# Kernel optimization log

Measured on AMD Instinct MI355X. Metric: run time of the kernel, lower is better.

Reference implementation:

```python
import jax, jax.numpy as jnp
import numpy as np

B, T, V, E_DIM, H = 1024, 512, 8, 32, 64  # batch, seq_len, num_actions, embed_dim, hidden_dim


def setup_inputs() -> dict:
    key = jax.random.key(0)
    ks = jax.random.split(key, 12)
    s = lambda k, shape: jax.random.normal(k, shape, dtype=jnp.float32) * 0.1
    return {
        "x": jax.random.randint(ks[0], (B, T), 0, V),
        "emb": s(ks[1], (V, E_DIM)),
        # PyTorch LSTM layer 0: weight_ih [4H, E], weight_hh [4H, H], biases [4H]
        "Wih0": s(ks[2], (4 * H, E_DIM)), "Whh0": s(ks[3], (4 * H, H)),
        "bih0": s(ks[4], (4 * H,)), "bhh0": s(ks[5], (4 * H,)),
        # layer 1: input size H
        "Wih1": s(ks[6], (4 * H, H)), "Whh1": s(ks[7], (4 * H, H)),
        "bih1": s(ks[8], (4 * H,)), "bhh1": s(ks[9], (4 * H,)),
        "Wfc": s(ks[10], (V, H)), "bfc": s(ks[11], (V,)),
    }


def _lstm_layer(x, Wih, Whh, bih, bhh):
    """Single LSTM layer, batch_first input x: [B, T, in] -> [B, T, H].
    PyTorch gate order: i, f, g, o."""
    Bsz = x.shape[0]
    Hd = Whh.shape[1]
    # precompute input contribution for all timesteps in one GEMM: [B, T, 4H]
    x_gates = jnp.einsum('bti,gi->btg', x, Wih) + bih + bhh

    def step(carry, xg):
        h, c = carry
        gates = xg + h @ Whh.T  # [B, 4H]
        i, f, g, o = jnp.split(gates, 4, axis=-1)
        i = jax.nn.sigmoid(i)
        f = jax.nn.sigmoid(f)
        g = jnp.tanh(g)
        o = jax.nn.sigmoid(o)
        c = f * c + i * g
        h = o * jnp.tanh(c)
        return (h, c), h

    h0 = jnp.zeros((Bsz, Hd), x.dtype)
    (_, _), hs = jax.lax.scan(step, (h0, h0), jnp.swapaxes(x_gates, 0, 1))
    return jnp.swapaxes(hs, 0, 1)  # [B, T, H]


def reference(x, emb, Wih0, Whh0, bih0, bhh0, Wih1, Whh1, bih1, bhh1, Wfc, bfc):
    # embedding lookup
    e = emb[x]  # [B, T, E]
    # 2-layer LSTM (dropout between layers / before fc is identity in eval mode)
    h1 = _lstm_layer(e, Wih0, Whh0, bih0, bhh0)
    h2 = _lstm_layer(h1, Wih1, Whh1, bih1, bhh1)
    last = h2[:, -1, :]  # [B, H]
    logits = last @ Wfc.T + bfc  # [B, V]
    return logits
```

## Files before the change

### kernel.cpp

```cpp
#include <hip/hip_runtime.h>

#define Bsz   1024
#define Tlen  512
#define VOC   8
#define EDIM  32
#define HDIM  64
#define G4    256
#define SEQB  4
#define NT    512
#define NBLK  (Bsz / SEQB)
#define ITERS 520

typedef _Float16 f16x8 __attribute__((ext_vector_type(8)));
typedef float    f32x4 __attribute__((ext_vector_type(4)));

__device__ __forceinline__ float ex2(float x) {
#if __has_builtin(__builtin_amdgcn_exp2f)
    return __builtin_amdgcn_exp2f(x);
#else
    return exp2f(x);
#endif
}
__device__ __forceinline__ float rcp_(float x) {
#if __has_builtin(__builtin_amdgcn_rcpf)
    return __builtin_amdgcn_rcpf(x);
#else
    return 1.0f / x;
#endif
}

__device__ __forceinline__ void cell_upd(float ai, float af, float ag, float ao,
                                         float& c, float& h) {
    const float K1 = 1.4426950408889634f;
    float ei = ex2(fminf(-K1 * ai, 60.0f));
    float ef = ex2(fminf(-K1 * af, 60.0f));
    float eg = ex2(fminf(-2.0f * K1 * ag, 60.0f));
    float eo = ex2(fminf(-K1 * ao, 60.0f));
    float di = 1.0f + ei, df = 1.0f + ef, dg = 1.0f + eg, dn = 1.0f + eo;
    float r1 = rcp_(di * df);
    float si = df * r1;
    float sf = di * r1;
    float r2 = rcp_(dg * dn);
    float tg = __builtin_fmaf(2.0f * dn, r2, -1.0f);
    float so = dg * r2;
    c = sf * c + si * tg;
    float ec = ex2(fminf(-2.0f * K1 * c, 60.0f));
    h = so * __builtin_fmaf(2.0f, rcp_(1.0f + ec), -1.0f);
}

__global__ void precompute_kernel(const float* __restrict__ emb,
                                  const float* __restrict__ Wih0,
                                  const float* __restrict__ bih0,
                                  const float* __restrict__ bhh0,
                                  const float* __restrict__ bih1,
                                  const float* __restrict__ bhh1,
                                  float* __restrict__ ws) {
    int g = threadIdx.x;
    int v = blockIdx.x;
    if (v < VOC) {
        float acc = bih0[g] + bhh0[g];
        #pragma unroll
        for (int e = 0; e < EDIM; ++e)
            acc += Wih0[g * EDIM + e] * emb[v * EDIM + e];
        const int q = g >> 6, c = g & 63;
        ws[(v * 64 + c) * 4 + q] = acc;
    } else {
        ws[VOC * G4 + g] = bih1[g] + bhh1[g];
    }
}

__device__ __forceinline__ f16x8 read_h_frag(const _Float16* hb, int kc, int l) {
    int off = kc * 512 + ((l * 8) ^ ((l & 3) << 7));
    return *(const f16x8*)(hb + off);
}
__device__ __forceinline__ void write_h(_Float16* hb, int r, int c, float v) {
    int off = (c >> 5) * 512 +
              (((((c & 31) >> 3) * 128) + r * 8 + (c & 7)) ^ ((r & 3) << 7));
    hb[off] = (_Float16)v;
}

#define MFMA8(A0, A1, W0, W1, C0, C1, C2, C3)                                   \
    C0 = __builtin_amdgcn_mfma_f32_16x16x32_f16(A0, W0[0], C0, 0, 0, 0);        \
    C1 = __builtin_amdgcn_mfma_f32_16x16x32_f16(A0, W0[1], C1, 0, 0, 0);        \
    C2 = __builtin_amdgcn_mfma_f32_16x16x32_f16(A0, W0[2], C2, 0, 0, 0);        \
    C3 = __builtin_amdgcn_mfma_f32_16x16x32_f16(A0, W0[3], C3, 0, 0, 0);        \
    C0 = __builtin_amdgcn_mfma_f32_16x16x32_f16(A1, W1[0], C0, 0, 0, 0);        \
    C1 = __builtin_amdgcn_mfma_f32_16x16x32_f16(A1, W1[1], C1, 0, 0, 0);        \
    C2 = __builtin_amdgcn_mfma_f32_16x16x32_f16(A1, W1[2], C2, 0, 0, 0);        \
    C3 = __builtin_amdgcn_mfma_f32_16x16x32_f16(A1, W1[3], C3, 0, 0, 0);

__global__ __launch_bounds__(NT)
void lstm_kernel(const int*   __restrict__ x,
                 const float* __restrict__ Whh0,
                 const float* __restrict__ Wih1,
                 const float* __restrict__ Whh1,
                 const float* __restrict__ Wfc,
                 const float* __restrict__ bfc,
                 const float* __restrict__ ws,
                 float* __restrict__ out) {
    __shared__ float4    stbl4[VOC * 64];
    __shared__ int       sxl[SEQB * Tlen];
    __shared__ _Float16  bbuf[2][1024];
    __shared__ _Float16  h1buf[2][1024];
    __shared__ float     pbuf[2][4][4][4][64];
    __shared__ float     sh1f[SEQB][HDIM + 1];

    const int tid  = threadIdx.x;
    const int b0   = blockIdx.x * SEQB;
    const int l    = tid & 63;
    const int wid  = tid >> 6;
    const bool isL1 = (wid >= 4);
    const int w    = wid & 3;
    const int l15  = l & 15;
    const int kbq  = (l >> 4) * 8;
    const int cq0  = 16 * w + l15;
    const int s    = l >> 4;
    const int r4   = 4 * s;

    for (int i = tid; i < VOC * 64; i += NT)
        stbl4[i] = ((const float4*)ws)[i];
    for (int i = tid; i < SEQB * Tlen; i += NT)
        sxl[i] = x[b0 * Tlen + i];
    for (int i = tid; i < 2 * 1024; i += NT) {
        ((_Float16*)bbuf)[i]  = (_Float16)0.0f;
        ((_Float16*)h1buf)[i] = (_Float16)0.0f;
    }

    f16x8 wA0[4], wA1[4], wI0[4], wI1[4], wH0[4], wH1[4];
    float b1q[4] = {0.0f, 0.0f, 0.0f, 0.0f};
    if (!isL1) {
        #pragma unroll
        for (int q = 0; q < 4; ++q) {
            const int cq = 64 * q + cq0;
            const float* p0 = Whh0 + cq * HDIM + kbq;
            const float* p1 = Whh0 + cq * HDIM + 32 + kbq;
            #pragma unroll
            for (int i = 0; i < 8; ++i) { wA0[q][i] = (_Float16)p0[i]; wA1[q][i] = (_Float16)p1[i]; }
        }
    } else {
        #pragma unroll
        for (int q = 0; q < 4; ++q) {
            const int cq = 64 * q + cq0;
            b1q[q] = ws[VOC * G4 + cq];
            const float* pi0 = Wih1 + cq * HDIM + kbq;
            const float* pi1 = Wih1 + cq * HDIM + 32 + kbq;
            const float* ph0 = Whh1 + cq * HDIM + kbq;
            const float* ph1 = Whh1 + cq * HDIM + 32 + kbq;
            #pragma unroll
            for (int i = 0; i < 8; ++i) {
                wI0[q][i] = (_Float16)pi0[i]; wI1[q][i] = (_Float16)pi1[i];
                wH0[q][i] = (_Float16)ph0[i]; wH1[q][i] = (_Float16)ph1[i];
            }
        }
    }

    float cst = 0.0f;
    __syncthreads();

    int tc = isL1 ? 0 : sxl[s * Tlen];

#define BODY(J)                                                                  \
    {                                                                            \
        const int k = kb + (J);                                                  \
        if (!isL1) {                                                             \
            if (k < Tlen) {                                                      \
                const _Float16* rb = bbuf[((k + 7) >> 2) & 1];                   \
                f16x8 a0 = read_h_frag(rb, 0, l);                                \
                f16x8 a1 = read_h_frag(rb, 1, l);                                \
                f32x4 tq = *(const f32x4*)&stbl4[tc * 64 + cq0];                 \
                f32x4 c0 = (f32x4)(0.0f), c1 = (f32x4)(0.0f);                    \
                f32x4 c2 = (f32x4)(0.0f), c3 = (f32x4)(0.0f);                    \
                MFMA8(a0, a1, wA0, wA1, c0, c1, c2, c3)                          \
                const int kn = (k + 1 < Tlen) ? (k + 1) : (Tlen - 1);            \
                const int tnext = sxl[s * Tlen + kn];                            \
                const int J0 = ((J) + 3) & 3;                                    \
                float ai = c0[J0] + tq[0];                                       \
                float af = c1[J0] + tq[1];                                       \
                float ag = c2[J0] + tq[2];                                       \
                float ao = c3[J0] + tq[3];                                       \
                float hv;                                                        \
                cell_upd(ai, af, ag, ao, cst, hv);                               \
                write_h(bbuf[(k >> 2) & 1], r4 + (J), cq0, hv);                  \
                tc = tnext;                                                      \
            }                                                                    \
        } else {                                                                 \
            if ((J) == 0 && k >= 4 && k <= Tlen) {                               \
                const int pb = ((k >> 2) + 1) & 1;                               \
                const _Float16* ib = bbuf[pb];                                   \
                f16x8 d0 = read_h_frag(ib, 0, l);                                \
                f16x8 d1 = read_h_frag(ib, 1, l);                                \
                f32x4 i0 = (f32x4)(0.0f), i1 = (f32x4)(0.0f);                    \
                f32x4 i2 = (f32x4)(0.0f), i3 = (f32x4)(0.0f);                    \
                MFMA8(d0, d1, wI0, wI1, i0, i1, i2, i3)                          \
                _Pragma("unroll")                                                \
                for (int jj = 0; jj < 4; ++jj) {                                 \
                    pbuf[pb][jj][w][0][l] = i0[jj];                              \
                    pbuf[pb][jj][w][1][l] = i1[jj];                              \
                    pbuf[pb][jj][w][2][l] = i2[jj];                              \
                    pbuf[pb][jj][w][3][l] = i3[jj];                              \
                }                                                                \
            }                                                                    \
            if (k >= 5 && k < Tlen + 5) {                                        \
                const int t = k - 5;                                             \
                const _Float16* hbp = h1buf[(t + 1) & 1];                        \
                f16x8 b0f = read_h_frag(hbp, 0, l);                              \
                f16x8 b1f = read_h_frag(hbp, 1, l);                              \
                f32x4 c0 = (f32x4)(0.0f), c1 = (f32x4)(0.0f);                    \
                f32x4 c2 = (f32x4)(0.0f), c3 = (f32x4)(0.0f);                    \
                MFMA8(b0f, b1f, wH0, wH1, c0, c1, c2, c3)                        \
                const int pr = (t >> 2) & 1;                                     \
                const int tm = ((J) + 3) & 3;                                    \
                float ai = c0[0] + pbuf[pr][tm][w][0][l] + b1q[0];               \
                float af = c1[0] + pbuf[pr][tm][w][1][l] + b1q[1];               \
                float ag = c2[0] + pbuf[pr][tm][w][2][l] + b1q[2];               \
                float ao = c3[0] + pbuf[pr][tm][w][3][l] + b1q[3];               \
                float hv;                                                        \
                cell_upd(ai, af, ag, ao, cst, hv);                               \
                if (t == Tlen - 1) sh1f[s][cq0] = hv;                            \
                else               write_h(h1buf[t & 1], r4, cq0, hv);           \
            }                                                                    \
        }                                                                        \
        __syncthreads();                                                         \
    }

    #pragma unroll 1
    for (int kb = 0; kb < ITERS; kb += 4) {
        BODY(0)
        BODY(1)
        BODY(2)
        BODY(3)
    }
#undef BODY

    if (tid < SEQB * VOC) {
        const int seq = tid >> 3, v = tid & 7;
        float acc2 = bfc[v];
        #pragma unroll
        for (int j = 0; j < HDIM; ++j)
            acc2 += Wfc[v * HDIM + j] * sh1f[seq][j];
        out[(b0 + seq) * VOC + v] = acc2;
    }
}

extern "C" void kernel_launch(void* const* d_in, const int* in_sizes, int n_in,
                              void* d_out, int out_size, void* d_ws, size_t ws_size,
                              hipStream_t stream) {
    const int*   x    = (const int*)  d_in[0];
    const float* emb  = (const float*)d_in[1];
    const float* Wih0 = (const float*)d_in[2];
    const float* Whh0 = (const float*)d_in[3];
    const float* bih0 = (const float*)d_in[4];
    const float* bhh0 = (const float*)d_in[5];
    const float* Wih1 = (const float*)d_in[6];
    const float* Whh1 = (const float*)d_in[7];
    const float* bih1 = (const float*)d_in[8];
    const float* bhh1 = (const float*)d_in[9];
    const float* Wfc  = (const float*)d_in[10];
    const float* bfc  = (const float*)d_in[11];
    float* out = (float*)d_out;
    float* ws  = (float*)d_ws;

    hipLaunchKernelGGL(precompute_kernel, dim3(VOC + 1), dim3(G4), 0, stream,
                       emb, Wih0, bih0, bhh0, bih1, bhh1, ws);
    hipLaunchKernelGGL(lstm_kernel, dim3(NBLK), dim3(NT), 0, stream,
                       x, Whh0, Wih1, Whh1, Wfc, bfc, ws, out);
}
```

Before: 213.1 us.

## Split each recurrence step into staggered MFMA and cell-update phases across layers

Each timestep of the fused two-layer LSTM loop is split into two barrier-separated phases. Layer-0 waves do their recurrent MFMA in phase A and their gate/cell update in phase B. Layer-1 waves do the reverse, with their pipeline delayed by one more step. The aim is to run one layer's matrix-core work alongside the other layer's transcendental-heavy cell update, so neither unit sits idle on the serial critical path. In exchange the loop has twice as many __syncthreads, and MFMA results must stay live in registers across the phase boundary.

```diff
diff --git a/kernel.cpp b/kernel.cpp
--- a/kernel.cpp
+++ b/kernel.cpp
@@ -155,11 +155,17 @@
     }
 
     float cst = 0.0f;
+    f32x4 l0c0 = (f32x4)(0.0f), l0c1 = (f32x4)(0.0f);
+    f32x4 l0c2 = (f32x4)(0.0f), l0c3 = (f32x4)(0.0f);
+    f32x4 tqc  = (f32x4)(0.0f);
+    int   tnc  = 0;
+    f32x4 hA0 = (f32x4)(0.0f), hA1 = (f32x4)(0.0f);
+    f32x4 hA2 = (f32x4)(0.0f), hA3 = (f32x4)(0.0f);
     __syncthreads();
 
     int tc = isL1 ? 0 : sxl[s * Tlen];
 
-#define BODY(J)                                                                  \
+#define BODYA(J)                                                                 \
     {                                                                            \
         const int k = kb + (J);                                                  \
         if (!isL1) {                                                             \
@@ -167,21 +173,46 @@
                 const _Float16* rb = bbuf[((k + 7) >> 2) & 1];                   \
                 f16x8 a0 = read_h_frag(rb, 0, l);                                \
                 f16x8 a1 = read_h_frag(rb, 1, l);                                \
-                f32x4 tq = *(const f32x4*)&stbl4[tc * 64 + cq0];                 \
+                tqc = *(const f32x4*)&stbl4[tc * 64 + cq0];                      \
                 f32x4 c0 = (f32x4)(0.0f), c1 = (f32x4)(0.0f);                    \
                 f32x4 c2 = (f32x4)(0.0f), c3 = (f32x4)(0.0f);                    \
                 MFMA8(a0, a1, wA0, wA1, c0, c1, c2, c3)                          \
+                l0c0 = c0; l0c1 = c1; l0c2 = c2; l0c3 = c3;                      \
                 const int kn = (k + 1 < Tlen) ? (k + 1) : (Tlen - 1);            \
-                const int tnext = sxl[s * Tlen + kn];                            \
+                tnc = sxl[s * Tlen + kn];                                        \
+            }                                                                    \
+        } else {                                                                 \
+            if (k >= 6 && k < Tlen + 6) {                                        \
+                const int t2 = k - 6;                                            \
+                const int pr = (t2 >> 2) & 1;                                    \
+                const int tm = ((J) + 2) & 3;                                    \
+                float ai = hA0[0] + pbuf[pr][tm][w][0][l] + b1q[0];              \
+                float af = hA1[0] + pbuf[pr][tm][w][1][l] + b1q[1];              \
+                float ag = hA2[0] + pbuf[pr][tm][w][2][l] + b1q[2];              \
+                float ao = hA3[0] + pbuf[pr][tm][w][3][l] + b1q[3];              \
+                float hv;                                                        \
+                cell_upd(ai, af, ag, ao, cst, hv);                               \
+                if (t2 == Tlen - 1) sh1f[s][cq0] = hv;                           \
+                else                write_h(h1buf[t2 & 1], r4, cq0, hv);         \
+            }                                                                    \
+        }                                                                        \
+        __syncthreads();                                                         \
+    }
+
+#define BODYB(J)                                                                 \
+    {                                                                            \
+        const int k = kb + (J);                                                  \
+        if (!isL1) {                                                             \
+            if (k < Tlen) {                                                      \
                 const int J0 = ((J) + 3) & 3;                                    \
-                float ai = c0[J0] + tq[0];                                       \
-                float af = c1[J0] + tq[1];                                       \
-                float ag = c2[J0] + tq[2];                                       \
-                float ao = c3[J0] + tq[3];                                       \
+                float ai = l0c0[J0] + tqc[0];                                    \
+                float af = l0c1[J0] + tqc[1];                                    \
+                float ag = l0c2[J0] + tqc[2];                                    \
+                float ao = l0c3[J0] + tqc[3];                                    \
                 float hv;                                                        \
                 cell_upd(ai, af, ag, ao, cst, hv);                               \
                 write_h(bbuf[(k >> 2) & 1], r4 + (J), cq0, hv);                  \
-                tc = tnext;                                                      \
+                tc = tnc;                                                        \
             }                                                                    \
         } else {                                                                 \
             if ((J) == 0 && k >= 4 && k <= Tlen) {                               \
@@ -208,16 +239,7 @@
                 f32x4 c0 = (f32x4)(0.0f), c1 = (f32x4)(0.0f);                    \
                 f32x4 c2 = (f32x4)(0.0f), c3 = (f32x4)(0.0f);                    \
                 MFMA8(b0f, b1f, wH0, wH1, c0, c1, c2, c3)                        \
-                const int pr = (t >> 2) & 1;                                     \
-                const int tm = ((J) + 3) & 3;                                    \
-                float ai = c0[0] + pbuf[pr][tm][w][0][l] + b1q[0];               \
-                float af = c1[0] + pbuf[pr][tm][w][1][l] + b1q[1];               \
-                float ag = c2[0] + pbuf[pr][tm][w][2][l] + b1q[2];               \
-                float ao = c3[0] + pbuf[pr][tm][w][3][l] + b1q[3];               \
-                float hv;                                                        \
-                cell_upd(ai, af, ag, ao, cst, hv);                               \
-                if (t == Tlen - 1) sh1f[s][cq0] = hv;                            \
-                else               write_h(h1buf[t & 1], r4, cq0, hv);           \
+                hA0 = c0; hA1 = c1; hA2 = c2; hA3 = c3;                          \
             }                                                                    \
         }                                                                        \
         __syncthreads();                                                         \
@@ -225,12 +247,13 @@
 
     #pragma unroll 1
     for (int kb = 0; kb < ITERS; kb += 4) {
-        BODY(0)
-        BODY(1)
-        BODY(2)
-        BODY(3)
-    }
-#undef BODY
+        BODYA(0) BODYB(0)
+        BODYA(1) BODYB(1)
+        BODYA(2) BODYB(2)
+        BODYA(3) BODYB(3)
+    }
+#undef BODYA
+#undef BODYB
 
     if (tid < SEQB * VOC) {
         const int seq = tid >> 3, v = tid & 7;
```

Result: slower. 264.0 us (+23.9%).
